# Kernel optimization log

Hardware: AMD Instinct MI355X
Metric: run time of the kernel (lower is better)

## Reference

```python
import jax, jax.numpy as jnp
import numpy as np

NUM_USERS = 100_000
NUM_JOBS = 100_000
N_NODES = NUM_USERS + NUM_JOBS
E = 3_200_000
D = 64  # embedding_dim == hidden_dim
B = 16_384


def setup_inputs() -> dict:
    key = jax.random.key(0)
    ks = jax.random.split(key, 10)
    edge_index = jax.random.randint(ks[0], (2, E), 0, N_NODES, dtype=jnp.int64)
    user_indices = jax.random.randint(ks[1], (B,), 0, NUM_USERS, dtype=jnp.int64)
    job_indices = jax.random.randint(ks[2], (B,), 0, NUM_JOBS, dtype=jnp.int64)
    # parameters (match reset_parameters: embeddings std=0.1, xavier pred, zero bias)
    user_emb_w = 0.1 * jax.random.normal(ks[3], (NUM_USERS, D), dtype=jnp.float32)
    job_emb_w = 0.1 * jax.random.normal(ks[4], (NUM_JOBS, D), dtype=jnp.float32)
    W1 = jax.random.normal(ks[5], (D, D), dtype=jnp.float32) / np.sqrt(D)
    b1 = jnp.zeros((D,), dtype=jnp.float32)
    W2 = jax.random.normal(ks[6], (D, D), dtype=jnp.float32) / np.sqrt(D)
    b2 = jnp.zeros((D,), dtype=jnp.float32)
    lim = np.sqrt(6.0 / (2 * D + 1))
    pred_w = jax.random.uniform(ks[7], (2 * D, 1), dtype=jnp.float32, minval=-lim, maxval=lim)
    pred_b = jnp.zeros((1,), dtype=jnp.float32)
    return {
        "edge_index": edge_index, "user_indices": user_indices, "job_indices": job_indices,
        "user_emb_w": user_emb_w, "job_emb_w": job_emb_w,
        "W1": W1, "b1": b1, "W2": W2, "b2": b2,
        "pred_w": pred_w, "pred_b": pred_b,
    }


def reference(edge_index, user_indices, job_indices, user_emb_w, job_emb_w, W1, b1, W2, b2, pred_w, pred_b):
    num_users = user_emb_w.shape[0]
    n = num_users + job_emb_w.shape[0]
    x = jnp.concatenate([user_emb_w, job_emb_w], axis=0)  # [N, D]

    # GCNConv (PyG defaults): add self-loops, symmetric D^-1/2 (A+I) D^-1/2 normalization
    loops = jnp.arange(n, dtype=edge_index.dtype)
    row = jnp.concatenate([edge_index[0], loops])  # source nodes
    col = jnp.concatenate([edge_index[1], loops])  # target nodes
    deg = jax.ops.segment_sum(jnp.ones_like(col, dtype=x.dtype), col, num_segments=n)
    dinv = jnp.where(deg > 0, jax.lax.rsqrt(jnp.maximum(deg, 1e-12)), 0.0)
    norm = dinv[row] * dinv[col]  # [E+N]

    def gcn_conv(h, W, b):
        h = h @ W                                   # [N, D]
        msg = h[row] * norm[:, None]                # gather + scale, [E+N, D]
        agg = jax.ops.segment_sum(msg, col, num_segments=n)  # scatter-add
        return agg + b

    x = jax.nn.relu(gcn_conv(x, W1, b1))  # dropout is identity at inference
    x = gcn_conv(x, W2, b2)

    user_emb = x[user_indices]                      # [B, D]
    job_emb = x[num_users + job_indices]            # [B, D]
    combined = jnp.concatenate([user_emb, job_emb], axis=1)  # [B, 2D]
    return (combined @ pred_w + pred_b)[:, 0]       # [B]
```

## Files before the change

kernel.cpp:

```cpp
#include <hip/hip_runtime.h>
#include <hip/hip_fp16.h>

#define D 64
#define BSHIFT 10
#define BMASK ((1 << BSHIFT) - 1)
#define NBUK_MAX 256
#define T_TILE 6144
#define EPT 24
#define CAP 20480

#if defined(__has_builtin)
#if __has_builtin(__builtin_amdgcn_fdot2)
#define HAVE_FDOT2 1
#endif
#endif

typedef _Float16 h2f __attribute__((ext_vector_type(2)));
typedef _Float16 half8v __attribute__((ext_vector_type(8)));
typedef float f4v __attribute__((ext_vector_type(4)));

__device__ __forceinline__ int wave_iscan(int v, int lane) {
#pragma unroll
    for (int off = 1; off < 64; off <<= 1) {
        int u = __shfl_up(v, off, 64);
        if (lane >= off) v += u;
    }
    return v;
}

__device__ __forceinline__ int block_escan(int v, int tid, int* wtot ) {
    int lane = tid & 63, w = tid >> 6;
    int inc = wave_iscan(v, lane);
    if (lane == 63) wtot[w] = inc;
    __syncthreads();
    int addv = 0;
#pragma unroll
    for (int q = 0; q < 4; q++) addv += (q < w) ? wtot[q] : 0;
    return inc - v + addv;
}

__device__ __forceinline__ float4 h4_to_f4(uint2 u) {
    __half2 a = *(__half2*)&u.x, b = *(__half2*)&u.y;
    float2 fa = __half22float2(a), fb = __half22float2(b);
    return make_float4(fa.x, fa.y, fb.x, fb.y);
}

__device__ __forceinline__ void acc_u2(float* acc, uint2 u) {
#ifdef HAVE_FDOT2
    h2f a0, a1;
    __builtin_memcpy(&a0, &u.x, 4);
    __builtin_memcpy(&a1, &u.y, 4);
    const h2f LO = {(_Float16)1.0f, (_Float16)0.0f};
    const h2f HI = {(_Float16)0.0f, (_Float16)1.0f};
    acc[0] = __builtin_amdgcn_fdot2(a0, LO, acc[0], false);
    acc[1] = __builtin_amdgcn_fdot2(a0, HI, acc[1], false);
    acc[2] = __builtin_amdgcn_fdot2(a1, LO, acc[2], false);
    acc[3] = __builtin_amdgcn_fdot2(a1, HI, acc[3], false);
#else
    float4 v = h4_to_f4(u);
    acc[0] += v.x; acc[1] += v.y; acc[2] += v.z; acc[3] += v.w;
#endif
}

__device__ __forceinline__ void acc_u4(float* acc, uint4 u) {
    uint2 a; a.x = u.x; a.y = u.y;
    uint2 b; b.x = u.z; b.y = u.w;
    acc_u2(acc, a);
    acc_u2(acc + 4, b);
}


__global__ __launch_bounds__(256) void k_bin(const int* __restrict__ row, const int* __restrict__ col,
                                             int E, int* __restrict__ bbase,
                                             unsigned* __restrict__ ebuf, int nbuk,
                                             const float* __restrict__ W1, const float* __restrict__ W2,
                                             __half* __restrict__ WT1, __half* __restrict__ WT2) {
    __shared__ int hist4[4][NBUK_MAX];
    __shared__ int sexcl[NBUK_MAX];
    __shared__ int cur4[4][NBUK_MAX];
    __shared__ int gbase[NBUK_MAX];
    __shared__ int wtot[4];
    __shared__ unsigned stage[T_TILE];
    __shared__ unsigned char sbuk[T_TILE];
    int tid = threadIdx.x;
    int w = tid >> 6;
    int tile0 = blockIdx.x * T_TILE;
    int cnt = min(T_TILE, E - tile0);

    if (blockIdx.x < 2) {
        const float* Ws = blockIdx.x ? W2 : W1;
        __half* Wd = blockIdx.x ? WT2 : WT1;
#pragma unroll
        for (int i = 0; i < 16; i++) {
            int f = i * 256 + tid;
            int k = f >> 6, c = f & 63;
            Wd[c * 64 + k] = __float2half(Ws[f]);
        }
    }

    unsigned pk[EPT];
    int bk[EPT];

#pragma unroll
    for (int q = 0; q < 4; q++) hist4[q][tid] = 0;
    __syncthreads();
#pragma unroll
    for (int j = 0; j < EPT / 4; j++) {
        int i4 = j * 1024 + tid * 4;
        if (i4 + 3 < cnt) {
            int4 r4 = *(const int4*)(row + tile0 + i4);
            int4 c4 = *(const int4*)(col + tile0 + i4);
            int rr[4] = {r4.x, r4.y, r4.z, r4.w};
            int cc[4] = {c4.x, c4.y, c4.z, c4.w};
#pragma unroll
            for (int q = 0; q < 4; q++) {
                int jj = j * 4 + q;
                bk[jj] = cc[q] >> BSHIFT;
                pk[jj] = ((unsigned)(cc[q] & BMASK) << 18) | (unsigned)rr[q];
                atomicAdd(&hist4[w][bk[jj]], 1);
            }
        } else {
#pragma unroll
            for (int q = 0; q < 4; q++) {
                int jj = j * 4 + q;
                int i = i4 + q;
                if (i < cnt) {
                    int r = row[tile0 + i];
                    int c = col[tile0 + i];
                    bk[jj] = c >> BSHIFT;
                    pk[jj] = ((unsigned)(c & BMASK) << 18) | (unsigned)r;
                    atomicAdd(&hist4[w][bk[jj]], 1);
                } else {
                    bk[jj] = -1;
                }
            }
        }
    }
    __syncthreads();

    int h0 = hist4[0][tid], h1 = hist4[1][tid], h2 = hist4[2][tid], h3 = hist4[3][tid];
    int v = h0 + h1 + h2 + h3;
    int excl = block_escan(v, tid, wtot);
    sexcl[tid] = excl;
    cur4[0][tid] = excl;
    cur4[1][tid] = excl + h0;
    cur4[2][tid] = excl + h0 + h1;
    cur4[3][tid] = excl + h0 + h1 + h2;
    gbase[tid] = (v > 0 && tid < nbuk) ? (tid * CAP + atomicAdd(&bbase[tid], v)) : 0;
    __syncthreads();

#pragma unroll
    for (int j = 0; j < EPT; j++) {
        if (bk[j] >= 0) {
            int p = atomicAdd(&cur4[w][bk[j]], 1);
            stage[p] = pk[j];
            sbuk[p] = (unsigned char)bk[j];
        }
    }
    __syncthreads();

    for (int i = tid; i < cnt; i += 256) {
        int b = sbuk[i];
        int gpos = gbase[b] + (i - sexcl[b]);
        ebuf[gpos] = stage[i];
    }
}


__global__ __launch_bounds__(256) void k_csr2a_conv(const unsigned* __restrict__ ebuf,
                                                    const int* __restrict__ bbase, int N, int nbuk,
                                                    int2* __restrict__ rps, float* __restrict__ dinv,
                                                    const float* __restrict__ xu, const float* __restrict__ xj,
                                                    int U, __half* __restrict__ h) {
    __shared__ int lcnt[1 << BSHIFT];
    __shared__ int wtot[4];
    int tid = threadIdx.x;

    if ((int)blockIdx.x >= nbuk) {
        int m0 = ((int)blockIdx.x - nbuk) * 128;
#pragma unroll
        for (int i = 0; i < 4; i++) {
            int slot = i * 256 + tid;
            int nl = slot >> 3, q = slot & 7;
            int nn = m0 + nl;
            if (nn < N) {
                const float* src = (nn < U) ? (xu + (size_t)nn * D) : (xj + (size_t)(nn - U) * D);
                float4 a = *(const float4*)(src + q * 8);
                float4 b = *(const float4*)(src + q * 8 + 4);
                __half2 p0 = __floats2half2_rn(a.x, a.y);
                __half2 p1 = __floats2half2_rn(a.z, a.w);
                __half2 p2 = __floats2half2_rn(b.x, b.y);
                __half2 p3 = __floats2half2_rn(b.z, b.w);
                uint4 st;
                st.x = *(unsigned*)&p0; st.y = *(unsigned*)&p1;
                st.z = *(unsigned*)&p2; st.w = *(unsigned*)&p3;
                *(uint4*)(h + (size_t)nn * D + q * 8) = st;
            }
        }
        return;
    }

    int c0 = blockIdx.x << BSHIFT;
    int nn = min(1 << BSHIFT, N - c0);
    int e0 = blockIdx.x * CAP, e1 = e0 + bbase[blockIdx.x];

    if (blockIdx.x == 0 && tid < 16) {
        uint2 z; z.x = 0u; z.y = 0u;
        *(uint2*)(h + (size_t)N * D + tid * 4) = z;
    }

    for (int i = tid; i < (1 << BSHIFT); i += 256) lcnt[i] = 0;
    __syncthreads();
    int len = e1 - e0;
    int nf = len & ~3;
    for (int j = tid * 4; j < nf; j += 1024) {
        uint4 v = *(const uint4*)(ebuf + e0 + j);
        atomicAdd(&lcnt[v.x >> 18], 1);
        atomicAdd(&lcnt[v.y >> 18], 1);
        atomicAdd(&lcnt[v.z >> 18], 1);
        atomicAdd(&lcnt[v.w >> 18], 1);
    }
    if (tid < (len - nf)) atomicAdd(&lcnt[ebuf[e0 + nf + tid] >> 18], 1);
    __syncthreads();

    int c[4]; int s = 0;
#pragma unroll
    for (int i = 0; i < 4; i++) { c[i] = lcnt[tid * 4 + i]; s += c[i]; }
    int run = block_escan(s, tid, wtot);
#pragma unroll
    for (int i = 0; i < 4; i++) {
        int idx = tid * 4 + i;
        if (idx < nn) {
            int st = e0 + run;
            rps[c0 + idx] = make_int2(st, st + c[i]);
            dinv[c0 + idx] = rsqrtf((float)(c[i] + 1));
        }
        run += c[i];
    }
}

__device__ __forceinline__ void stage_Wt(const __half* __restrict__ WTg, __half* __restrict__ Wt, int tid) {
#pragma unroll
    for (int i = 0; i < 2; i++) {
        int f = (i * 256 + tid) * 8;
        int c = f >> 6, k = f & 63;
        *(half8v*)(Wt + c * 72 + k) = *(const half8v*)(WTg + f);
    }
}


__global__ __launch_bounds__(256) void k_csr2b_gemm1(const unsigned* __restrict__ ebuf,
                                                     const int2* __restrict__ rps,
                                                     const int* __restrict__ bbase,
                                                     int N, int nbuk, int* __restrict__ srcs,
                                                     const __half* __restrict__ WT1,
                                                     const float* __restrict__ dinv, __half* __restrict__ h) {
    __shared__ __align__(16) __half Xh[64 * 72];
    __shared__ __align__(16) __half Wt[64 * 72];
    int tid = threadIdx.x;
    if ((int)blockIdx.x < nbuk) {
        int* lcur = (int*)Xh;
        int c0 = blockIdx.x << BSHIFT;
        int e0 = blockIdx.x * CAP, e1 = e0 + bbase[blockIdx.x];
        for (int i = tid; i < (1 << BSHIFT); i += 256)
            lcur[i] = (c0 + i < N) ? rps[c0 + i].x : 0;
        __syncthreads();
        int len = e1 - e0;
        int nf = len & ~3;
        for (int j = tid * 4; j < nf; j += 1024) {
            uint4 v = *(const uint4*)(ebuf + e0 + j);
            int p0 = atomicAdd(&lcur[v.x >> 18], 1); srcs[p0] = (int)(v.x & 0x3ffffu);
            int p1 = atomicAdd(&lcur[v.y >> 18], 1); srcs[p1] = (int)(v.y & 0x3ffffu);
            int p2 = atomicAdd(&lcur[v.z >> 18], 1); srcs[p2] = (int)(v.z & 0x3ffffu);
            int p3 = atomicAdd(&lcur[v.w >> 18], 1); srcs[p3] = (int)(v.w & 0x3ffffu);
        }
        if (tid < (len - nf)) {
            unsigned pk = ebuf[e0 + nf + tid];
            int p = atomicAdd(&lcur[pk >> 18], 1);
            srcs[p] = (int)(pk & 0x3ffffu);
        }
    } else {
        int n0 = ((int)blockIdx.x - nbuk) * 64;
        stage_Wt(WT1, Wt, tid);
#pragma unroll
        for (int i = 0; i < 2; i++) {
            int slot = i * 256 + tid;
            int nl = slot >> 3, q = slot & 7;
            int nn = n0 + nl;
            uint4 st; st.x = 0u; st.y = 0u; st.z = 0u; st.w = 0u;
            if (nn < N) st = *(const uint4*)(h + (size_t)nn * D + q * 8);
            *(uint4*)(Xh + nl * 72 + q * 8) = st;
        }
        __syncthreads();

        int lane = tid & 63;
        int wv = tid >> 6;
        int n16 = lane & 15, quad = lane >> 4;
        const __half* Xw = Xh + (wv * 16) * 72;
        half8v a0 = *(const half8v*)(Xw + n16 * 72 + quad * 8);
        half8v a1 = *(const half8v*)(Xw + n16 * 72 + quad * 8 + 32);
        f4v acc[4];
#pragma unroll
        for (int ct = 0; ct < 4; ct++) {
            acc[ct] = (f4v){0.f, 0.f, 0.f, 0.f};
            const __half* wp = Wt + (ct * 16 + n16) * 72;
            half8v b0 = *(const half8v*)(wp + quad * 8);
            half8v b1 = *(const half8v*)(wp + quad * 8 + 32);
            acc[ct] = __builtin_amdgcn_mfma_f32_16x16x32_f16(a0, b0, acc[ct], 0, 0, 0);
            acc[ct] = __builtin_amdgcn_mfma_f32_16x16x32_f16(a1, b1, acc[ct], 0, 0, 0);
        }
#pragma unroll
        for (int r = 0; r < 4; r++) {
            int node = n0 + wv * 16 + quad * 4 + r;
            if (node < N) {
                float dv = dinv[node];
#pragma unroll
                for (int ct = 0; ct < 4; ct++)
                    h[(size_t)node * D + ct * 16 + n16] = __float2half(acc[ct][r] * dv);
            }
        }
    }
}


__device__ __forceinline__ void gather16(float* acc, const __half* __restrict__ hs,
                                         const int2* __restrict__ rps,
                                         const int* __restrict__ srcs,
                                         int node, int N, int g, int t) {
    const __half* hp = hs + t * 8;
    int2 r = rps[node];
    int e0 = r.x, deg = r.y - r.x;
    int base = g * 8;
    for (int cb = 0; cb < deg; cb += 16) {
        int svA = (cb + t < deg) ? srcs[e0 + cb + t] : N;
        int svB = (cb + 8 + t < deg) ? srcs[e0 + cb + 8 + t] : N;
        int sA[8], sB[8];
#pragma unroll
        for (int q = 0; q < 8; q++) sA[q] = __shfl(svA, base + q, 64);
#pragma unroll
        for (int q = 0; q < 8; q++) sB[q] = __shfl(svB, base + q, 64);
        uint4 uA[8], uB[8];
#pragma unroll
        for (int q = 0; q < 8; q++) uA[q] = *(const uint4*)(hp + (size_t)sA[q] * D);
#pragma unroll
        for (int q = 0; q < 8; q++) uB[q] = *(const uint4*)(hp + (size_t)sB[q] * D);
#pragma unroll
        for (int q = 0; q < 8; q++) acc_u4(acc, uA[q]);
#pragma unroll
        for (int q = 0; q < 8; q++) acc_u4(acc, uB[q]);
    }
}


__global__ __launch_bounds__(256) void k_agg_gemm2(const __half* __restrict__ hs, const float* __restrict__ dinv,
                                                   const int2* __restrict__ rps, const int* __restrict__ srcs,
                                                   const float* __restrict__ bias, const __half* __restrict__ WT2,
                                                   const float* __restrict__ pw, int N,
                                                   float* __restrict__ zu, float* __restrict__ zj) {
    __shared__ __align__(16) __half Xh[64 * 72];
    __shared__ __align__(16) __half Wt[64 * 72];
    int tid = threadIdx.x;
    int lane = tid & 63;
    int w = tid >> 6;
    int g = lane >> 3, t = lane & 7;
    int n0 = blockIdx.x * 64;

    stage_Wt(WT2, Wt, tid);

    float4 ba = *(const float4*)(bias + t * 8);
    float4 bb = *(const float4*)(bias + t * 8 + 4);
#pragma unroll
    for (int rr = 0; rr < 2; rr++) {
        int nl = w * 16 + rr * 8 + g;
        int node = n0 + nl;
        uint4 st; st.x = 0u; st.y = 0u; st.z = 0u; st.w = 0u;
        if (node < N) {
            float acc[8] = {0.f, 0.f, 0.f, 0.f, 0.f, 0.f, 0.f, 0.f};
            gather16(acc, hs, rps, srcs, node, N, g, t);
            uint4 su = *(const uint4*)(hs + (size_t)node * D + t * 8);
            float4 sa = h4_to_f4(make_uint2(su.x, su.y));
            float4 sb = h4_to_f4(make_uint2(su.z, su.w));
            float dv = dinv[node];
            float o0 = fmaxf((acc[0] + sa.x) * dv + ba.x, 0.f);
            float o1 = fmaxf((acc[1] + sa.y) * dv + ba.y, 0.f);
            float o2 = fmaxf((acc[2] + sa.z) * dv + ba.z, 0.f);
            float o3 = fmaxf((acc[3] + sa.w) * dv + ba.w, 0.f);
            float o4 = fmaxf((acc[4] + sb.x) * dv + bb.x, 0.f);
            float o5 = fmaxf((acc[5] + sb.y) * dv + bb.y, 0.f);
            float o6 = fmaxf((acc[6] + sb.z) * dv + bb.z, 0.f);
            float o7 = fmaxf((acc[7] + sb.w) * dv + bb.w, 0.f);
            __half2 p0 = __floats2half2_rn(o0, o1);
            __half2 p1 = __floats2half2_rn(o2, o3);
            __half2 p2 = __floats2half2_rn(o4, o5);
            __half2 p3 = __floats2half2_rn(o6, o7);
            st.x = *(unsigned*)&p0; st.y = *(unsigned*)&p1;
            st.z = *(unsigned*)&p2; st.w = *(unsigned*)&p3;
        }
        *(uint4*)(Xh + nl * 72 + t * 8) = st;
    }
    __syncthreads();

    int wv = w;
    int n16 = lane & 15, quad = lane >> 4;
    const __half* Xw = Xh + (wv * 16) * 72;
    half8v a0 = *(const half8v*)(Xw + n16 * 72 + quad * 8);
    half8v a1 = *(const half8v*)(Xw + n16 * 72 + quad * 8 + 32);
    f4v acc[4];
    float pwu_r[4], pwj_r[4];
#pragma unroll
    for (int ct = 0; ct < 4; ct++) {
        pwu_r[ct] = pw[ct * 16 + n16];
        pwj_r[ct] = pw[64 + ct * 16 + n16];
        acc[ct] = (f4v){0.f, 0.f, 0.f, 0.f};
        const __half* wp = Wt + (ct * 16 + n16) * 72;
        half8v b0 = *(const half8v*)(wp + quad * 8);
        half8v b1 = *(const half8v*)(wp + quad * 8 + 32);
        acc[ct] = __builtin_amdgcn_mfma_f32_16x16x32_f16(a0, b0, acc[ct], 0, 0, 0);
        acc[ct] = __builtin_amdgcn_mfma_f32_16x16x32_f16(a1, b1, acc[ct], 0, 0, 0);
    }
#pragma unroll
    for (int r = 0; r < 4; r++) {
        int node = n0 + wv * 16 + quad * 4 + r;
        float dv = (node < N) ? dinv[node] : 0.0f;
        float su = acc[0][r] * pwu_r[0] + acc[1][r] * pwu_r[1]
                 + acc[2][r] * pwu_r[2] + acc[3][r] * pwu_r[3];
        float sj = acc[0][r] * pwj_r[0] + acc[1][r] * pwj_r[1]
                 + acc[2][r] * pwj_r[2] + acc[3][r] * pwj_r[3];
        su += __shfl_xor(su, 1, 64); sj += __shfl_xor(sj, 1, 64);
        su += __shfl_xor(su, 2, 64); sj += __shfl_xor(sj, 2, 64);
        su += __shfl_xor(su, 4, 64); sj += __shfl_xor(sj, 4, 64);
        su += __shfl_xor(su, 8, 64); sj += __shfl_xor(sj, 8, 64);
        if (n16 == 0 && node < N) {
            zu[node] = su * dv;
            zj[node] = sj * dv;
        }
    }
}


__global__ __launch_bounds__(256) void k_pred(const float* __restrict__ zu, const float* __restrict__ zj,
                                              const float* __restrict__ dinv,
                                              const int2* __restrict__ rps, const int* __restrict__ srcs,
                                              const float* __restrict__ b2, const float* __restrict__ pw,
                                              const float* __restrict__ pb,
                                              const int* __restrict__ uidx, const int* __restrict__ jidx,
                                              int U, int N, int B, float* __restrict__ out) {
    int tid = threadIdx.x;
    int lane = tid & 63;
    int g = lane >> 3, t = lane & 7;
    int pair = blockIdx.x * 16 + (tid >> 6) * 4 + (g >> 1);
    if (pair >= B) return;
    int side = g & 1;
    int c = side ? (U + jidx[pair]) : uidx[pair];
    const float* zt = side ? zj : zu;

    float4 b2a = *(const float4*)(b2 + t * 8);
    float4 b2b = *(const float4*)(b2 + t * 8 + 4);
    float4 wa = *(const float4*)(pw + side * 64 + t * 8);
    float4 wb = *(const float4*)(pw + side * 64 + t * 8 + 4);
    float cpart = b2a.x * wa.x + b2a.y * wa.y + b2a.z * wa.z + b2a.w * wa.w
                + b2b.x * wb.x + b2b.y * wb.y + b2b.z * wb.z + b2b.w * wb.w;

    int2 r = rps[c];
    int deg = r.y - r.x;
    float s = 0.f;
    for (int cb = 0; cb < deg; cb += 8) {
        if (cb + t < deg) s += zt[srcs[r.x + cb + t]];
    }
    s += __shfl_xor(s, 1, 64); cpart += __shfl_xor(cpart, 1, 64);
    s += __shfl_xor(s, 2, 64); cpart += __shfl_xor(cpart, 2, 64);
    s += __shfl_xor(s, 4, 64); cpart += __shfl_xor(cpart, 4, 64);

    float val = (s + zt[c]) * dinv[c] + cpart;
    val += __shfl_xor(val, 8, 64);
    if ((lane & 15) == 0) out[pair] = val + pb[0];
}


extern "C" void kernel_launch(void* const* d_in, const int* in_sizes, int n_in,
                              void* d_out, int out_size, void* d_ws, size_t ws_size,
                              hipStream_t stream) {
    const int*   edge = (const int*)d_in[0];
    const int*   uidx = (const int*)d_in[1];
    const int*   jidx = (const int*)d_in[2];
    const float* xu   = (const float*)d_in[3];
    const float* xj   = (const float*)d_in[4];
    const float* W1   = (const float*)d_in[5];
    const float* b1   = (const float*)d_in[6];
    const float* W2   = (const float*)d_in[7];
    const float* b2   = (const float*)d_in[8];
    const float* pw   = (const float*)d_in[9];
    const float* pb   = (const float*)d_in[10];
    float* out = (float*)d_out;

    int E = in_sizes[0] / 2;
    int B = in_sizes[1];
    int U = in_sizes[3] / D;
    int J = in_sizes[4] / D;
    int N = U + J;
    int nbuk = (N + (1 << BSHIFT) - 1) >> BSHIFT;
    int nconv = (N + 127) / 128;
    const int* row = edge;
    const int* col = edge + E;

    char* p = (char*)d_ws;
    auto alloc = [&](size_t bytes) -> void* {
        void* q = (void*)p;
        p += (bytes + 255) / 256 * 256;
        return q;
    };
    size_t capsz = (size_t)nbuk * CAP * 4;
    int*      bbase = (int*)alloc(256 * 4);
    int2*     rps   = (int2*)alloc((size_t)N * 8);
    float*    dinv  = (float*)alloc((size_t)N * 4);
    int*      srcs  = (int*)alloc(capsz);
    __half*   h     = (__half*)alloc((size_t)(N + 1) * D * 2);
    unsigned* ebuf  = (unsigned*)alloc(capsz);
    float*    zu    = (float*)alloc((size_t)N * 4);
    float*    zj    = (float*)alloc((size_t)N * 4);
    __half*   WT1   = (__half*)alloc((size_t)D * D * 2);
    __half*   WT2   = (__half*)alloc((size_t)D * D * 2);

    hipMemsetAsync(bbase, 0, 256 * 4, stream);

    k_bin<<<(E + T_TILE - 1) / T_TILE, 256, 0, stream>>>(row, col, E, bbase, ebuf, nbuk,
                                                         W1, W2, WT1, WT2);

    k_csr2a_conv<<<nbuk + nconv, 256, 0, stream>>>(ebuf, bbase, N, nbuk, rps, dinv,
                                                   xu, xj, U, h);

    k_csr2b_gemm1<<<nbuk + (N + 63) / 64, 256, 0, stream>>>(ebuf, rps, bbase, N, nbuk, srcs,
                                                            WT1, dinv, h);

    k_agg_gemm2<<<(N + 63) / 64, 256, 0, stream>>>(h, dinv, rps, srcs, b1, WT2, pw, N, zu, zj);

    k_pred<<<(B + 15) / 16, 256, 0, stream>>>(zu, zj, dinv, rps, srcs, b2, pw, pb,
                                              uidx, jidx, U, N, B, out);
}
```

Measured before the change: 242.4 us.

## Move fp16 embedding conversion into binning kernel and shrink gather batch to 8

```diff
diff --git a/kernel.cpp b/kernel.cpp
--- a/kernel.cpp
+++ b/kernel.cpp
@@ -70,11 +70,14 @@
 }
 
 
-__global__ __launch_bounds__(256) void k_bin(const int* __restrict__ row, const int* __restrict__ col,
-                                             int E, int* __restrict__ bbase,
-                                             unsigned* __restrict__ ebuf, int nbuk,
-                                             const float* __restrict__ W1, const float* __restrict__ W2,
-                                             __half* __restrict__ WT1, __half* __restrict__ WT2) {
+__global__ __launch_bounds__(256) void k_bin_conv(const int* __restrict__ row, const int* __restrict__ col,
+                                                  int E, int nbin, int* __restrict__ bbase,
+                                                  unsigned* __restrict__ ebuf, int nbuk,
+                                                  const float* __restrict__ xu, const float* __restrict__ xj,
+                                                  int U, int N,
+                                                  const float* __restrict__ W1, const float* __restrict__ W2,
+                                                  __half* __restrict__ WT1, __half* __restrict__ WT2,
+                                                  __half* __restrict__ h) {
     __shared__ int hist4[4][NBUK_MAX];
     __shared__ int sexcl[NBUK_MAX];
     __shared__ int cur4[4][NBUK_MAX];
@@ -83,101 +86,9 @@
     __shared__ unsigned stage[T_TILE];
     __shared__ unsigned char sbuk[T_TILE];
     int tid = threadIdx.x;
-    int w = tid >> 6;
-    int tile0 = blockIdx.x * T_TILE;
-    int cnt = min(T_TILE, E - tile0);
-
-    if (blockIdx.x < 2) {
-        const float* Ws = blockIdx.x ? W2 : W1;
-        __half* Wd = blockIdx.x ? WT2 : WT1;
-#pragma unroll
-        for (int i = 0; i < 16; i++) {
-            int f = i * 256 + tid;
-            int k = f >> 6, c = f & 63;
-            Wd[c * 64 + k] = __float2half(Ws[f]);
-        }
-    }
-
-    unsigned pk[EPT];
-    int bk[EPT];
-
-#pragma unroll
-    for (int q = 0; q < 4; q++) hist4[q][tid] = 0;
-    __syncthreads();
-#pragma unroll
-    for (int j = 0; j < EPT / 4; j++) {
-        int i4 = j * 1024 + tid * 4;
-        if (i4 + 3 < cnt) {
-            int4 r4 = *(const int4*)(row + tile0 + i4);
-            int4 c4 = *(const int4*)(col + tile0 + i4);
-            int rr[4] = {r4.x, r4.y, r4.z, r4.w};
-            int cc[4] = {c4.x, c4.y, c4.z, c4.w};
-#pragma unroll
-            for (int q = 0; q < 4; q++) {
-                int jj = j * 4 + q;
-                bk[jj] = cc[q] >> BSHIFT;
-                pk[jj] = ((unsigned)(cc[q] & BMASK) << 18) | (unsigned)rr[q];
-                atomicAdd(&hist4[w][bk[jj]], 1);
-            }
-        } else {
-#pragma unroll
-            for (int q = 0; q < 4; q++) {
-                int jj = j * 4 + q;
-                int i = i4 + q;
-                if (i < cnt) {
-                    int r = row[tile0 + i];
-                    int c = col[tile0 + i];
-                    bk[jj] = c >> BSHIFT;
-                    pk[jj] = ((unsigned)(c & BMASK) << 18) | (unsigned)r;
-                    atomicAdd(&hist4[w][bk[jj]], 1);
-                } else {
-                    bk[jj] = -1;
-                }
-            }
-        }
-    }
-    __syncthreads();
-
-    int h0 = hist4[0][tid], h1 = hist4[1][tid], h2 = hist4[2][tid], h3 = hist4[3][tid];
-    int v = h0 + h1 + h2 + h3;
-    int excl = block_escan(v, tid, wtot);
-    sexcl[tid] = excl;
-    cur4[0][tid] = excl;
-    cur4[1][tid] = excl + h0;
-    cur4[2][tid] = excl + h0 + h1;
-    cur4[3][tid] = excl + h0 + h1 + h2;
-    gbase[tid] = (v > 0 && tid < nbuk) ? (tid * CAP + atomicAdd(&bbase[tid], v)) : 0;
-    __syncthreads();
-
-#pragma unroll
-    for (int j = 0; j < EPT; j++) {
-        if (bk[j] >= 0) {
-            int p = atomicAdd(&cur4[w][bk[j]], 1);
-            stage[p] = pk[j];
-            sbuk[p] = (unsigned char)bk[j];
-        }
-    }
-    __syncthreads();
-
-    for (int i = tid; i < cnt; i += 256) {
-        int b = sbuk[i];
-        int gpos = gbase[b] + (i - sexcl[b]);
-        ebuf[gpos] = stage[i];
-    }
-}
-
-
-__global__ __launch_bounds__(256) void k_csr2a_conv(const unsigned* __restrict__ ebuf,
-                                                    const int* __restrict__ bbase, int N, int nbuk,
-                                                    int2* __restrict__ rps, float* __restrict__ dinv,
-                                                    const float* __restrict__ xu, const float* __restrict__ xj,
-                                                    int U, __half* __restrict__ h) {
-    __shared__ int lcnt[1 << BSHIFT];
-    __shared__ int wtot[4];
-    int tid = threadIdx.x;
-
-    if ((int)blockIdx.x >= nbuk) {
-        int m0 = ((int)blockIdx.x - nbuk) * 128;
+
+    if ((int)blockIdx.x >= nbin) {
+        int m0 = ((int)blockIdx.x - nbin) * 128;
 #pragma unroll
         for (int i = 0; i < 4; i++) {
             int slot = i * 256 + tid;
@@ -200,6 +111,97 @@
         return;
     }
 
+    int w = tid >> 6;
+    int tile0 = blockIdx.x * T_TILE;
+    int cnt = min(T_TILE, E - tile0);
+
+    if (blockIdx.x < 2) {
+        const float* Ws = blockIdx.x ? W2 : W1;
+        __half* Wd = blockIdx.x ? WT2 : WT1;
+#pragma unroll
+        for (int i = 0; i < 16; i++) {
+            int f = i * 256 + tid;
+            int k = f >> 6, c = f & 63;
+            Wd[c * 64 + k] = __float2half(Ws[f]);
+        }
+    }
+
+    unsigned pk[EPT];
+    int bk[EPT];
+
+#pragma unroll
+    for (int q = 0; q < 4; q++) hist4[q][tid] = 0;
+    __syncthreads();
+#pragma unroll
+    for (int j = 0; j < EPT / 4; j++) {
+        int i4 = j * 1024 + tid * 4;
+        if (i4 + 3 < cnt) {
+            int4 r4 = *(const int4*)(row + tile0 + i4);
+            int4 c4 = *(const int4*)(col + tile0 + i4);
+            int rr[4] = {r4.x, r4.y, r4.z, r4.w};
+            int cc[4] = {c4.x, c4.y, c4.z, c4.w};
+#pragma unroll
+            for (int q = 0; q < 4; q++) {
+                int jj = j * 4 + q;
+                bk[jj] = cc[q] >> BSHIFT;
+                pk[jj] = ((unsigned)(cc[q] & BMASK) << 18) | (unsigned)rr[q];
+                atomicAdd(&hist4[w][bk[jj]], 1);
+            }
+        } else {
+#pragma unroll
+            for (int q = 0; q < 4; q++) {
+                int jj = j * 4 + q;
+                int i = i4 + q;
+                if (i < cnt) {
+                    int r = row[tile0 + i];
+                    int c = col[tile0 + i];
+                    bk[jj] = c >> BSHIFT;
+                    pk[jj] = ((unsigned)(c & BMASK) << 18) | (unsigned)r;
+                    atomicAdd(&hist4[w][bk[jj]], 1);
+                } else {
+                    bk[jj] = -1;
+                }
+            }
+        }
+    }
+    __syncthreads();
+
+    int h0 = hist4[0][tid], h1 = hist4[1][tid], h2 = hist4[2][tid], h3 = hist4[3][tid];
+    int v = h0 + h1 + h2 + h3;
+    int excl = block_escan(v, tid, wtot);
+    sexcl[tid] = excl;
+    cur4[0][tid] = excl;
+    cur4[1][tid] = excl + h0;
+    cur4[2][tid] = excl + h0 + h1;
+    cur4[3][tid] = excl + h0 + h1 + h2;
+    gbase[tid] = (v > 0 && tid < nbuk) ? (tid * CAP + atomicAdd(&bbase[tid], v)) : 0;
+    __syncthreads();
+
+#pragma unroll
+    for (int j = 0; j < EPT; j++) {
+        if (bk[j] >= 0) {
+            int p = atomicAdd(&cur4[w][bk[j]], 1);
+            stage[p] = pk[j];
+            sbuk[p] = (unsigned char)bk[j];
+        }
+    }
+    __syncthreads();
+
+    for (int i = tid; i < cnt; i += 256) {
+        int b = sbuk[i];
+        int gpos = gbase[b] + (i - sexcl[b]);
+        ebuf[gpos] = stage[i];
+    }
+}
+
+
+__global__ __launch_bounds__(256) void k_csr2a(const unsigned* __restrict__ ebuf,
+                                               const int* __restrict__ bbase, int N,
+                                               int2* __restrict__ rps, float* __restrict__ dinv,
+                                               __half* __restrict__ h) {
+    __shared__ int lcnt[1 << BSHIFT];
+    __shared__ int wtot[4];
+    int tid = threadIdx.x;
     int c0 = blockIdx.x << BSHIFT;
     int nn = min(1 << BSHIFT, N - c0);
     int e0 = blockIdx.x * CAP, e1 = e0 + bbase[blockIdx.x];
@@ -323,31 +325,40 @@
 }
 
 
-__device__ __forceinline__ void gather16(float* acc, const __half* __restrict__ hs,
-                                         const int2* __restrict__ rps,
-                                         const int* __restrict__ srcs,
-                                         int node, int N, int g, int t) {
+__device__ __forceinline__ void gather8(float* acc, const __half* __restrict__ hs,
+                                        const int2* __restrict__ rps,
+                                        const int* __restrict__ srcs,
+                                        int node, int N, int g, int t) {
     const __half* hp = hs + t * 8;
     int2 r = rps[node];
     int e0 = r.x, deg = r.y - r.x;
-    int base = g * 8;
-    for (int cb = 0; cb < deg; cb += 16) {
-        int svA = (cb + t < deg) ? srcs[e0 + cb + t] : N;
-        int svB = (cb + 8 + t < deg) ? srcs[e0 + cb + 8 + t] : N;
-        int sA[8], sB[8];
-#pragma unroll
-        for (int q = 0; q < 8; q++) sA[q] = __shfl(svA, base + q, 64);
-#pragma unroll
-        for (int q = 0; q < 8; q++) sB[q] = __shfl(svB, base + q, 64);
-        uint4 uA[8], uB[8];
-#pragma unroll
-        for (int q = 0; q < 8; q++) uA[q] = *(const uint4*)(hp + (size_t)sA[q] * D);
-#pragma unroll
-        for (int q = 0; q < 8; q++) uB[q] = *(const uint4*)(hp + (size_t)sB[q] * D);
-#pragma unroll
-        for (int q = 0; q < 8; q++) acc_u4(acc, uA[q]);
-#pragma unroll
-        for (int q = 0; q < 8; q++) acc_u4(acc, uB[q]);
+    for (int cb = 0; cb < deg; cb += 8) {
+        int sv = (cb + t < deg) ? srcs[e0 + cb + t] : N;
+        int base = g * 8;
+        int s0 = __shfl(sv, base + 0, 64);
+        int s1 = __shfl(sv, base + 1, 64);
+        int s2 = __shfl(sv, base + 2, 64);
+        int s3 = __shfl(sv, base + 3, 64);
+        int s4 = __shfl(sv, base + 4, 64);
+        int s5 = __shfl(sv, base + 5, 64);
+        int s6 = __shfl(sv, base + 6, 64);
+        int s7 = __shfl(sv, base + 7, 64);
+        uint4 u0 = *(const uint4*)(hp + (size_t)s0 * D);
+        uint4 u1 = *(const uint4*)(hp + (size_t)s1 * D);
+        uint4 u2 = *(const uint4*)(hp + (size_t)s2 * D);
+        uint4 u3 = *(const uint4*)(hp + (size_t)s3 * D);
+        uint4 u4 = *(const uint4*)(hp + (size_t)s4 * D);
+        uint4 u5 = *(const uint4*)(hp + (size_t)s5 * D);
+        uint4 u6 = *(const uint4*)(hp + (size_t)s6 * D);
+        uint4 u7 = *(const uint4*)(hp + (size_t)s7 * D);
+        acc_u4(acc, u0);
+        acc_u4(acc, u1);
+        acc_u4(acc, u2);
+        acc_u4(acc, u3);
+        acc_u4(acc, u4);
+        acc_u4(acc, u5);
+        acc_u4(acc, u6);
+        acc_u4(acc, u7);
     }
 }
 
@@ -376,7 +387,7 @@
         uint4 st; st.x = 0u; st.y = 0u; st.z = 0u; st.w = 0u;
         if (node < N) {
             float acc[8] = {0.f, 0.f, 0.f, 0.f, 0.f, 0.f, 0.f, 0.f};
-            gather16(acc, hs, rps, srcs, node, N, g, t);
+            gather8(acc, hs, rps, srcs, node, N, g, t);
             uint4 su = *(const uint4*)(hs + (size_t)node * D + t * 8);
             float4 sa = h4_to_f4(make_uint2(su.x, su.y));
             float4 sb = h4_to_f4(make_uint2(su.z, su.w));
@@ -499,6 +510,7 @@
     int J = in_sizes[4] / D;
     int N = U + J;
     int nbuk = (N + (1 << BSHIFT) - 1) >> BSHIFT;
+    int nbin = (E + T_TILE - 1) / T_TILE;
     int nconv = (N + 127) / 128;
     const int* row = edge;
     const int* col = edge + E;
@@ -523,11 +535,10 @@
 
     hipMemsetAsync(bbase, 0, 256 * 4, stream);
 
-    k_bin<<<(E + T_TILE - 1) / T_TILE, 256, 0, stream>>>(row, col, E, bbase, ebuf, nbuk,
-                                                         W1, W2, WT1, WT2);
-
-    k_csr2a_conv<<<nbuk + nconv, 256, 0, stream>>>(ebuf, bbase, N, nbuk, rps, dinv,
-                                                   xu, xj, U, h);
+    k_bin_conv<<<nbin + nconv, 256, 0, stream>>>(row, col, E, nbin, bbase, ebuf, nbuk,
+                                                 xu, xj, U, N, W1, W2, WT1, WT2, h);
+
+    k_csr2a<<<nbuk, 256, 0, stream>>>(ebuf, bbase, N, rps, dinv, h);
 
     k_csr2b_gemm1<<<nbuk + (N + 63) / 64, 256, 0, stream>>>(ebuf, rps, bbase, N, nbuk, srcs,
                                                             WT1, dinv, h);
```

New measurement: 237.6 us. -2.0%, faster.
